# Kernel optimization log

Measured on AMD Instinct MI355X. Metric: run time of the kernel, lower is better.

Reference implementation:

```python
import jax, jax.numpy as jnp
import numpy as np


def setup_inputs() -> dict:
    key = jax.random.key(0)
    k_x, k_q, k_k, k_v = jax.random.split(key, 4)
    seq_len, d_in, d_out = 4096, 1024, 1024
    x = jax.random.normal(k_x, (seq_len, d_in), dtype=jnp.float32)
    # torch nn.Linear weights are [d_out, d_in]; applied as x @ W.T
    scale = 1.0 / np.sqrt(d_in)
    Wq = jax.random.uniform(k_q, (d_out, d_in), jnp.float32, -scale, scale)
    Wk = jax.random.uniform(k_k, (d_out, d_in), jnp.float32, -scale, scale)
    Wv = jax.random.uniform(k_v, (d_out, d_in), jnp.float32, -scale, scale)
    return {"x": x, "Wq": Wq, "Wk": Wk, "Wv": Wv}


def reference(x, Wq, Wk, Wv):
    # x: [S, d_in]; Wq/Wk/Wv: [d_out, d_in]
    queries = x @ Wq.T          # [S, d_out]
    keys = x @ Wk.T             # [S, d_out]
    values = x @ Wv.T           # [S, d_out]
    d_k = keys.shape[-1]
    attn_scores = queries @ keys.T                      # [S, S]
    attn_weights = jax.nn.softmax(attn_scores / jnp.sqrt(jnp.float32(d_k)), axis=-1)
    S = attn_scores.shape[0]
    tril = jnp.tril(jnp.ones((S, S), dtype=attn_weights.dtype))
    masked = tril * attn_weights
    masked_norm = masked / jnp.sum(masked, axis=-1, keepdims=True)
    context_vec = masked_norm @ values                  # [S, d_out]
    return context_vec
```

## Files before the change

### kernel.cpp

```cpp
#include <hip/hip_runtime.h>
#include <hip/hip_bf16.h>


typedef __bf16 bf16_t;
typedef __bf16 bf16x4v __attribute__((ext_vector_type(4)));
typedef __bf16 bf16x8 __attribute__((ext_vector_type(8)));
typedef float f32x4 __attribute__((ext_vector_type(4)));
typedef unsigned char u8;
typedef long long i64_t;

#define AS1 __attribute__((address_space(1)))
#define AS3 __attribute__((address_space(3)))

__device__ __forceinline__ void async_copy16(const void* g, void* l) {
    __builtin_amdgcn_global_load_lds((AS1 void*)(g), (AS3 void*)(l), 16, 0, 0);
}

__device__ __forceinline__ u8 f32_to_fp8(float v) {
    return (u8)(__builtin_amdgcn_cvt_pk_fp8_f32(v, v, 0, false) & 0xff);
}

__device__ __forceinline__ void store_conv(float* p, float v) { *p = v; }
__device__ __forceinline__ void store_conv(bf16_t* p, float v) { *p = (bf16_t)v; }
__device__ __forceinline__ void store_conv(u8* p, float v) { *p = f32_to_fp8(v); }

__device__ __forceinline__ float sum32(const float* p) {
    const f32x4* v = (const f32x4*)p;
    float s = 0.f;
#pragma unroll
    for (int u = 0; u < 8; ++u) {
        f32x4 a = v[u];
        s += a[0] + a[1] + a[2] + a[3];
    }
    return s;
}

template <int EPI, typename OutT>
__device__ __forceinline__ void gemm_tile_bf16(const bf16_t* __restrict__ A, int lda,
                                               const bf16_t* __restrict__ B, int ldb,
                                               OutT* __restrict__ C, int ldc,
                                               int kb0, int kb1, float alpha,
                                               bf16_t* __restrict__ As,
                                               bf16_t* __restrict__ Bs,
                                               const float* __restrict__ inv) {
    constexpr int BK = 64;
    const int tid = threadIdx.x;
    const int lane = tid & 63, wave = tid >> 6;
    const int wm = wave >> 1, wn = wave & 1;
    const int q = lane >> 4, l16 = lane & 15;

    f32x4 acc[4][4] = {};

    const bf16_t* aSrc[4];
    const bf16_t* bSrc[4];
    int ldsOff[4];
#pragma unroll
    for (int it = 0; it < 4; ++it) {
        int c = it * 256 + tid;
        int r = c >> 3, b = c & 7;
        int sb = b ^ (r & 7);
        aSrc[it] = A + (size_t)r * lda + sb * 8;
        bSrc[it] = B + (size_t)r * ldb + sb * 8;
        ldsOff[it] = c * 8;
    }

    for (int kb = kb0; kb < kb1; ++kb) {
        const int k0 = kb * BK;
#pragma unroll
        for (int it = 0; it < 4; ++it) async_copy16(aSrc[it] + k0, &As[ldsOff[it]]);
#pragma unroll
        for (int it = 0; it < 4; ++it) async_copy16(bSrc[it] + k0, &Bs[ldsOff[it]]);
        __syncthreads();

#pragma unroll
        for (int k2 = 0; k2 < 2; ++k2) {
            bf16x8 af[4], bfr[4];
#pragma unroll
            for (int mt = 0; mt < 4; ++mt) {
                int m = wm * 64 + mt * 16 + l16;
                int blk = (k2 * 4 + q) ^ (m & 7);
                af[mt] = *(const bf16x8*)&As[m * BK + blk * 8];
            }
#pragma unroll
            for (int nt = 0; nt < 4; ++nt) {
                int nn = wn * 64 + nt * 16 + l16;
                int blk = (k2 * 4 + q) ^ (nn & 7);
                bfr[nt] = *(const bf16x8*)&Bs[nn * BK + blk * 8];
            }
#pragma unroll
            for (int mt = 0; mt < 4; ++mt)
#pragma unroll
                for (int nt = 0; nt < 4; ++nt)
                    acc[mt][nt] = __builtin_amdgcn_mfma_f32_16x16x32_bf16(
                        af[mt], bfr[nt], acc[mt][nt], 0, 0, 0);
        }
        __syncthreads();
    }

    const int row0 = wm * 64, col0 = wn * 64;
#pragma unroll
    for (int mt = 0; mt < 4; ++mt)
#pragma unroll
        for (int nt = 0; nt < 4; ++nt)
#pragma unroll
            for (int r = 0; r < 4; ++r) {
                int lr = row0 + mt * 16 + q * 4 + r;
                float v = acc[mt][nt][r];
                v = (EPI == 2) ? v * inv[lr] : v * alpha;
                store_conv(&C[(size_t)lr * ldc + col0 + nt * 16 + l16], v);
            }
}

__device__ __forceinline__ void scores_tile_fp8(const u8* __restrict__ A, int lda,
                                                const u8* __restrict__ B, int ldb,
                                                bf16_t* __restrict__ C, int ldc,
                                                float alpha,
                                                u8* __restrict__ As, u8* __restrict__ Bs,
                                                float* __restrict__ partial,
                                                int gr0, int gc0,
                                                float* __restrict__ sred) {
    const int tid = threadIdx.x;
    const int lane = tid & 63, wave = tid >> 6;
    const int wm = wave >> 1, wn = wave & 1;
    const int q = lane >> 4, l16 = lane & 15;

    f32x4 acc[4][4] = {};

    const u8* aSrc[4];
    const u8* bSrc[4];
    int ldsOff[4];
#pragma unroll
    for (int it = 0; it < 4; ++it) {
        int c = it * 256 + tid;
        int r = c >> 3, b = c & 7;
        int sb = b ^ (r & 7);
        aSrc[it] = A + (size_t)r * lda + sb * 16;
        bSrc[it] = B + (size_t)r * ldb + sb * 16;
        ldsOff[it] = c * 16;
    }

    for (int kb = 0; kb < 8; ++kb) {
        const int k0 = kb * 128;
#pragma unroll
        for (int it = 0; it < 4; ++it) async_copy16(aSrc[it] + k0, &As[ldsOff[it]]);
#pragma unroll
        for (int it = 0; it < 4; ++it) async_copy16(bSrc[it] + k0, &Bs[ldsOff[it]]);
        __syncthreads();

#pragma unroll
        for (int k2 = 0; k2 < 4; ++k2) {
            i64_t af[4], bfr[4];
            const int cb = 2 * k2 + (q >> 1), co = (q & 1) * 8;
#pragma unroll
            for (int mt = 0; mt < 4; ++mt) {
                int m = wm * 64 + mt * 16 + l16;
                af[mt] = *(const i64_t*)&As[m * 128 + ((cb ^ (m & 7)) << 4) + co];
            }
#pragma unroll
            for (int nt = 0; nt < 4; ++nt) {
                int nn = wn * 64 + nt * 16 + l16;
                bfr[nt] = *(const i64_t*)&Bs[nn * 128 + ((cb ^ (nn & 7)) << 4) + co];
            }
#pragma unroll
            for (int mt = 0; mt < 4; ++mt)
#pragma unroll
                for (int nt = 0; nt < 4; ++nt)
                    acc[mt][nt] = __builtin_amdgcn_mfma_f32_16x16x32_fp8_fp8(
                        af[mt], bfr[nt], acc[mt][nt], 0, 0, 0);
        }
        __syncthreads();
    }

    const int row0 = wm * 64, col0 = wn * 64;
    float esum[4][4];
#pragma unroll
    for (int mt = 0; mt < 4; ++mt)
#pragma unroll
        for (int r = 0; r < 4; ++r) esum[mt][r] = 0.f;
#pragma unroll
    for (int mt = 0; mt < 4; ++mt)
#pragma unroll
        for (int nt = 0; nt < 4; ++nt)
#pragma unroll
            for (int r = 0; r < 4; ++r) {
                int lr = row0 + mt * 16 + q * 4 + r;
                int lc = col0 + nt * 16 + l16;
                float p = (gc0 + lc > gr0 + lr) ? 0.f : __expf(acc[mt][nt][r] * alpha);
                esum[mt][r] += p;
                C[(size_t)lr * ldc + lc] = (bf16_t)p;
            }
#pragma unroll
    for (int mt = 0; mt < 4; ++mt)
#pragma unroll
        for (int r = 0; r < 4; ++r) {
#pragma unroll
            for (int off = 1; off < 16; off <<= 1)
                esum[mt][r] += __shfl_xor(esum[mt][r], off, 64);
            if (l16 == 0) sred[(row0 + mt * 16 + q * 4 + r) * 2 + wn] = esum[mt][r];
        }
    __syncthreads();
    if (tid < 128) partial[(size_t)tid * 32] = sred[tid * 2] + sred[tid * 2 + 1];
}

__global__ __launch_bounds__(256) void k_qkv(const bf16_t* __restrict__ xb,
                                             const bf16_t* __restrict__ wqk,
                                             u8* __restrict__ qk) {
    __shared__ __attribute__((aligned(16))) bf16_t As[128 * 64];
    __shared__ __attribute__((aligned(16))) bf16_t Bs[128 * 64];
    int b = blockIdx.x;
    int bm = b & 31, bn = b >> 5;
    gemm_tile_bf16<0, u8>(xb + (size_t)bm * 128 * 1024, 1024,
                          wqk + (size_t)bn * 128 * 1024, 1024,
                          qk + (size_t)bm * 128 * 2048 + bn * 128, 2048,
                          0, 16, 1.f, As, Bs, nullptr);
}

__global__ __launch_bounds__(256) void k_sv(const bf16_t* __restrict__ xb,
                                            const bf16_t* __restrict__ wvb,
                                            const u8* __restrict__ qk,
                                            bf16_t* __restrict__ vt,
                                            bf16_t* __restrict__ P,
                                            float* __restrict__ rowsum_part) {
    __shared__ __attribute__((aligned(16))) char smem[33 * 1024 + 1024];
    int b = blockIdx.x;
    if (b < 256) {
        bf16_t* As = (bf16_t*)smem;
        bf16_t* Bs = (bf16_t*)(smem + 16384);
        int bm = b & 7, bn = b >> 3;
        gemm_tile_bf16<0, bf16_t>(wvb + (size_t)bm * 128 * 1024, 1024,
                                  xb + (size_t)bn * 128 * 1024, 1024,
                                  vt + (size_t)bm * 128 * 4096 + bn * 128, 4096,
                                  0, 16, 1.f, As, Bs, nullptr);
        return;
    }
    u8* As = (u8*)smem;
    u8* Bs = (u8*)(smem + 16384);
    float* sred = (float*)(smem + 32768);
    int t = b - 256;
    int bm = (int)((sqrtf(8.f * (float)t + 1.f) - 1.f) * 0.5f);
    while (bm * (bm + 1) / 2 > t) --bm;
    while ((bm + 1) * (bm + 2) / 2 <= t) ++bm;
    int bn = t - bm * (bm + 1) / 2;
    scores_tile_fp8(qk + (size_t)bm * 128 * 2048, 2048,
                    qk + 1024 + (size_t)bn * 128 * 2048, 2048,
                    P + (size_t)bm * 128 * 4096 + bn * 128, 4096,
                    0.03125f, As, Bs,
                    rowsum_part + (size_t)bm * 128 * 32 + bn,
                    bm * 128, bn * 128, sred);
    if (bn == bm) {
        float* rp = rowsum_part + (size_t)bm * 128 * 32;
        int tid = threadIdx.x;
        for (int r = tid >> 4; r < 128; r += 16)
            for (int u = bm + 1 + (tid & 15); u < 32; u += 16)
                rp[r * 32 + u] = 0.f;
    }
}

__global__ __launch_bounds__(256) void k_pv(const bf16_t* __restrict__ P,
                                            const bf16_t* __restrict__ vt,
                                            const float* __restrict__ rowsum_part,
                                            float* __restrict__ out,
                                            float* __restrict__ partials) {
    __shared__ __attribute__((aligned(16))) bf16_t As[128 * 64];
    __shared__ __attribute__((aligned(16))) bf16_t Bs[128 * 64];
    __shared__ float sInv[128];
    int b = blockIdx.x;
    int bn = b & 7, g = b >> 3;
    int bm, s, ns;
    if (g < 8)       { bm = g;                 s = 0;            ns = 1; }
    else if (g < 24) { bm = 8 + (g - 8) / 2;   s = (g - 8) % 2;  ns = 2; }
    else if (g < 48) { bm = 16 + (g - 24) / 3; s = (g - 24) % 3; ns = 3; }
    else             { bm = 24 + (g - 48) / 4; s = (g - 48) % 4; ns = 4; }
    int nk = 2 * (bm + 1);
    int kb0 = s * nk / ns;
    int kb1 = (s + 1) * nk / ns;

    const bf16_t* A = P + (size_t)bm * 128 * 4096;
    const bf16_t* B = vt + (size_t)bn * 128 * 4096;
    if (ns == 1) {
        int tid = threadIdx.x;
        if (tid < 128)
            sInv[tid] = 1.f / sum32(rowsum_part + (size_t)(bm * 128 + tid) * 32);
        gemm_tile_bf16<2, float>(A, 4096, B, 4096,
                                 out + (size_t)bm * 128 * 1024 + bn * 128, 1024,
                                 kb0, kb1, 1.f, As, Bs, sInv);
    } else {
        int cum = (bm < 16) ? (bm - 8) * 2
                : (bm < 24) ? 16 + (bm - 16) * 3
                            : 40 + (bm - 24) * 4;
        gemm_tile_bf16<0, float>(A, 4096, B, 4096,
                                 partials + ((size_t)(cum + s) * 8 + bn) * 16384, 128,
                                 kb0, kb1, 1.f, As, Bs, nullptr);
    }
}

__global__ __launch_bounds__(256) void k_reduce(const float* __restrict__ partials,
                                                const float* __restrict__ rowsum_part,
                                                float* __restrict__ out) {
    int b = blockIdx.x;
    int t = b % 192, p = b / 192;
    int bm = t % 24 + 8, bn = t / 24;
    int ns = (bm < 16) ? 2 : (bm < 24) ? 3 : 4;
    int cum = (bm < 16) ? (bm - 8) * 2
            : (bm < 24) ? 16 + (bm - 16) * 3
                        : 40 + (bm - 24) * 4;
    __shared__ float sInv[8];
    int tid = threadIdx.x;
    if (tid < 8) {
        int row = bm * 128 + p * 8 + tid;
        sInv[tid] = 1.f / sum32(rowsum_part + (size_t)row * 32);
    }
    __syncthreads();

    int idx = p * 1024 + tid * 4;
    int lr = idx >> 7, lc = idx & 127;
    float sx = 0.f, sy = 0.f, sz = 0.f, sw = 0.f;
    for (int u = 0; u < ns; ++u) {
        const float4 v = *(const float4*)(partials + ((size_t)(cum + u) * 8 + bn) * 16384 + idx);
        sx += v.x; sy += v.y; sz += v.z; sw += v.w;
    }
    float inv = sInv[lr - p * 8];
    float4 o = {sx * inv, sy * inv, sz * inv, sw * inv};
    *(float4*)(out + (size_t)(bm * 128 + lr) * 1024 + bn * 128 + lc) = o;
}

__global__ __launch_bounds__(256) void cast_to_bf16(const float* __restrict__ x,
                                                    const float* __restrict__ Wq,
                                                    const float* __restrict__ Wk,
                                                    const float* __restrict__ Wv,
                                                    bf16_t* __restrict__ xb,
                                                    bf16_t* __restrict__ wqk,
                                                    bf16_t* __restrict__ wv) {
    const int NX = (4096 * 1024) / 4;
    const int NW = (1024 * 1024) / 4;
    int idx = blockIdx.x * 256 + threadIdx.x;
    const float* src;
    bf16_t* dst;
    int off;
    if (idx < NX) {
        src = x; dst = xb; off = idx;
    } else if (idx < NX + NW) {
        src = Wq; dst = wqk; off = idx - NX;
    } else if (idx < NX + 2 * NW) {
        src = Wk; dst = wqk + (size_t)NW * 4; off = idx - NX - NW;
    } else {
        src = Wv; dst = wv; off = idx - NX - 2 * NW;
    }
    float4 f = ((const float4*)src)[off];
    bf16x4v o;
    o.x = (bf16_t)f.x; o.y = (bf16_t)f.y; o.z = (bf16_t)f.z; o.w = (bf16_t)f.w;
    *(bf16x4v*)(dst + (size_t)off * 4) = o;
}

extern "C" void kernel_launch(void* const* d_in, const int* in_sizes, int n_in,
                              void* d_out, int out_size, void* d_ws, size_t ws_size,
                              hipStream_t stream) {
    (void)in_sizes; (void)n_in; (void)out_size; (void)ws_size;
    const float* x  = (const float*)d_in[0];
    const float* Wq = (const float*)d_in[1];
    const float* Wk = (const float*)d_in[2];
    const float* Wv = (const float*)d_in[3];
    float* out = (float*)d_out;

    char* ws = (char*)d_ws;
    bf16_t* xb   = (bf16_t*)(ws + (size_t)0);
    bf16_t* wqk  = (bf16_t*)(ws + ((size_t)8 << 20));
    bf16_t* wvb  = (bf16_t*)(ws + ((size_t)12 << 20));
    u8*     qk   = (u8*)(ws + ((size_t)14 << 20));
    bf16_t* vt   = (bf16_t*)(ws + ((size_t)22 << 20));
    bf16_t* P    = (bf16_t*)(ws + ((size_t)30 << 20));
    float* rowsp = (float*)(ws + ((size_t)62 << 20));
    float* parts = (float*)(ws + ((size_t)64 << 20));

    cast_to_bf16<<<7168, 256, 0, stream>>>(x, Wq, Wk, Wv, xb, wqk, wvb);

    k_qkv<<<512, 256, 0, stream>>>(xb, wqk, qk);

    k_sv<<<784, 256, 0, stream>>>(xb, wvb, qk, vt, P, rowsp);

    k_pv<<<640, 256, 0, stream>>>(P, vt, rowsp, out, parts);
    k_reduce<<<3072, 256, 0, stream>>>(parts, rowsp, out);
}
```

Baseline: 188.8 us.

## Double-buffer LDS tiles in GEMM kernels and stage epilogue stores through LDS

The bf16 and fp8 GEMM tile routines now prefetch the next K-block into a second LDS buffer while computing on the current one, so global loads overlap with MFMA work and one barrier per iteration is removed. Epilogues write results into swizzled LDS and then issue coalesced 16-byte global stores instead of scattered scalar stores. LDS per block grows to 64 KB, which may lower occupancy. A wait on the async copies is also dropped, since only the end-of-iteration barrier orders the prefetch.

```diff
diff --git a/kernel.cpp b/kernel.cpp
--- a/kernel.cpp
+++ b/kernel.cpp
@@ -40,10 +40,11 @@
                                                const bf16_t* __restrict__ B, int ldb,
                                                OutT* __restrict__ C, int ldc,
                                                int kb0, int kb1, float alpha,
-                                               bf16_t* __restrict__ As,
-                                               bf16_t* __restrict__ Bs,
+                                               char* __restrict__ smem,
                                                const float* __restrict__ inv) {
     constexpr int BK = 64;
+    bf16_t* As = (bf16_t*)smem;
+    bf16_t* Bs = (bf16_t*)(smem + 32768);
     const int tid = threadIdx.x;
     const int lane = tid & 63, wave = tid >> 6;
     const int wm = wave >> 1, wn = wave & 1;
@@ -64,14 +65,27 @@
         ldsOff[it] = c * 8;
     }
 
+    {
+        const int k0 = kb0 * BK;
+#pragma unroll
+        for (int it = 0; it < 4; ++it) async_copy16(aSrc[it] + k0, &As[ldsOff[it]]);
+#pragma unroll
+        for (int it = 0; it < 4; ++it) async_copy16(bSrc[it] + k0, &Bs[ldsOff[it]]);
+    }
+    __syncthreads();
+
+    int cur = 0;
     for (int kb = kb0; kb < kb1; ++kb) {
-        const int k0 = kb * BK;
-#pragma unroll
-        for (int it = 0; it < 4; ++it) async_copy16(aSrc[it] + k0, &As[ldsOff[it]]);
-#pragma unroll
-        for (int it = 0; it < 4; ++it) async_copy16(bSrc[it] + k0, &Bs[ldsOff[it]]);
-        __syncthreads();
-
+        if (kb + 1 < kb1) {
+            const int k0 = (kb + 1) * BK;
+            const int boff = (cur ^ 1) * 8192;
+#pragma unroll
+            for (int it = 0; it < 4; ++it) async_copy16(aSrc[it] + k0, &As[boff + ldsOff[it]]);
+#pragma unroll
+            for (int it = 0; it < 4; ++it) async_copy16(bSrc[it] + k0, &Bs[boff + ldsOff[it]]);
+        }
+        const bf16_t* Ab = As + cur * 8192;
+        const bf16_t* Bb = Bs + cur * 8192;
 #pragma unroll
         for (int k2 = 0; k2 < 2; ++k2) {
             bf16x8 af[4], bfr[4];
@@ -79,13 +93,13 @@
             for (int mt = 0; mt < 4; ++mt) {
                 int m = wm * 64 + mt * 16 + l16;
                 int blk = (k2 * 4 + q) ^ (m & 7);
-                af[mt] = *(const bf16x8*)&As[m * BK + blk * 8];
+                af[mt] = *(const bf16x8*)&Ab[m * BK + blk * 8];
             }
 #pragma unroll
             for (int nt = 0; nt < 4; ++nt) {
                 int nn = wn * 64 + nt * 16 + l16;
                 int blk = (k2 * 4 + q) ^ (nn & 7);
-                bfr[nt] = *(const bf16x8*)&Bs[nn * BK + blk * 8];
+                bfr[nt] = *(const bf16x8*)&Bb[nn * BK + blk * 8];
             }
 #pragma unroll
             for (int mt = 0; mt < 4; ++mt)
@@ -95,8 +109,11 @@
                         af[mt], bfr[nt], acc[mt][nt], 0, 0, 0);
         }
         __syncthreads();
-    }
-
+        cur ^= 1;
+    }
+
+    constexpr int S = (int)sizeof(OutT);
+    constexpr int RB = 128 * S;
     const int row0 = wm * 64, col0 = wn * 64;
 #pragma unroll
     for (int mt = 0; mt < 4; ++mt)
@@ -105,20 +122,33 @@
 #pragma unroll
             for (int r = 0; r < 4; ++r) {
                 int lr = row0 + mt * 16 + q * 4 + r;
+                int lc = col0 + nt * 16 + l16;
                 float v = acc[mt][nt][r];
                 v = (EPI == 2) ? v * inv[lr] : v * alpha;
-                store_conv(&C[(size_t)lr * ldc + col0 + nt * 16 + l16], v);
-            }
+                int cb = (lc * S) >> 4;
+                int sw = cb ^ ((lr >> 2) & 7);
+                store_conv((OutT*)(smem + lr * RB + (sw << 4) + ((lc * S) & 15)), v);
+            }
+    __syncthreads();
+#pragma unroll
+    for (int p = 0; p < 4 * S; ++p) {
+        int g = p * 4096 + tid * 16;
+        int r = g / RB;
+        int wb = g & (RB - 1);
+        int sc = (wb >> 4) ^ ((r >> 2) & 7);
+        f32x4 val = *(const f32x4*)(smem + r * RB + (sc << 4));
+        *(f32x4*)((char*)C + (size_t)r * ((size_t)ldc * S) + wb) = val;
+    }
 }
 
 __device__ __forceinline__ void scores_tile_fp8(const u8* __restrict__ A, int lda,
                                                 const u8* __restrict__ B, int ldb,
                                                 bf16_t* __restrict__ C, int ldc,
-                                                float alpha,
-                                                u8* __restrict__ As, u8* __restrict__ Bs,
+                                                float alpha, char* __restrict__ smem,
                                                 float* __restrict__ partial,
-                                                int gr0, int gc0,
-                                                float* __restrict__ sred) {
+                                                int gr0, int gc0) {
+    u8* As = (u8*)smem;
+    u8* Bs = (u8*)(smem + 32768);
     const int tid = threadIdx.x;
     const int lane = tid & 63, wave = tid >> 6;
     const int wm = wave >> 1, wn = wave & 1;
@@ -139,14 +169,26 @@
         ldsOff[it] = c * 16;
     }
 
+    {
+#pragma unroll
+        for (int it = 0; it < 4; ++it) async_copy16(aSrc[it], &As[ldsOff[it]]);
+#pragma unroll
+        for (int it = 0; it < 4; ++it) async_copy16(bSrc[it], &Bs[ldsOff[it]]);
+    }
+    __syncthreads();
+
+    int cur = 0;
     for (int kb = 0; kb < 8; ++kb) {
-        const int k0 = kb * 128;
-#pragma unroll
-        for (int it = 0; it < 4; ++it) async_copy16(aSrc[it] + k0, &As[ldsOff[it]]);
-#pragma unroll
-        for (int it = 0; it < 4; ++it) async_copy16(bSrc[it] + k0, &Bs[ldsOff[it]]);
-        __syncthreads();
-
+        if (kb < 7) {
+            const int k0 = (kb + 1) * 128;
+            const int boff = (cur ^ 1) * 16384;
+#pragma unroll
+            for (int it = 0; it < 4; ++it) async_copy16(aSrc[it] + k0, &As[boff + ldsOff[it]]);
+#pragma unroll
+            for (int it = 0; it < 4; ++it) async_copy16(bSrc[it] + k0, &Bs[boff + ldsOff[it]]);
+        }
+        const u8* Ab = As + cur * 16384;
+        const u8* Bb = Bs + cur * 16384;
 #pragma unroll
         for (int k2 = 0; k2 < 4; ++k2) {
             i64_t af[4], bfr[4];
@@ -154,12 +196,12 @@
 #pragma unroll
             for (int mt = 0; mt < 4; ++mt) {
                 int m = wm * 64 + mt * 16 + l16;
-                af[mt] = *(const i64_t*)&As[m * 128 + ((cb ^ (m & 7)) << 4) + co];
+                af[mt] = *(const i64_t*)&Ab[m * 128 + ((cb ^ (m & 7)) << 4) + co];
             }
 #pragma unroll
             for (int nt = 0; nt < 4; ++nt) {
                 int nn = wn * 64 + nt * 16 + l16;
-                bfr[nt] = *(const i64_t*)&Bs[nn * 128 + ((cb ^ (nn & 7)) << 4) + co];
+                bfr[nt] = *(const i64_t*)&Bb[nn * 128 + ((cb ^ (nn & 7)) << 4) + co];
             }
 #pragma unroll
             for (int mt = 0; mt < 4; ++mt)
@@ -169,8 +211,10 @@
                         af[mt], bfr[nt], acc[mt][nt], 0, 0, 0);
         }
         __syncthreads();
-    }
-
+        cur ^= 1;
+    }
+
+    float* sred = (float*)(smem + 32768);
     const int row0 = wm * 64, col0 = wn * 64;
     float esum[4][4];
 #pragma unroll
@@ -185,9 +229,10 @@
             for (int r = 0; r < 4; ++r) {
                 int lr = row0 + mt * 16 + q * 4 + r;
                 int lc = col0 + nt * 16 + l16;
-                float p = (gc0 + lc > gr0 + lr) ? 0.f : __expf(acc[mt][nt][r] * alpha);
-                esum[mt][r] += p;
-                C[(size_t)lr * ldc + lc] = (bf16_t)p;
+                float pe = (gc0 + lc > gr0 + lr) ? 0.f : __expf(acc[mt][nt][r] * alpha);
+                esum[mt][r] += pe;
+                int sw = (lc >> 3) ^ ((lr >> 2) & 7);
+                *(bf16_t*)(smem + lr * 256 + (sw << 4) + ((lc * 2) & 15)) = (bf16_t)pe;
             }
 #pragma unroll
     for (int mt = 0; mt < 4; ++mt)
@@ -199,20 +244,28 @@
             if (l16 == 0) sred[(row0 + mt * 16 + q * 4 + r) * 2 + wn] = esum[mt][r];
         }
     __syncthreads();
+#pragma unroll
+    for (int p = 0; p < 8; ++p) {
+        int g = p * 4096 + tid * 16;
+        int r = g >> 8;
+        int wb = g & 255;
+        int sc = (wb >> 4) ^ ((r >> 2) & 7);
+        f32x4 val = *(const f32x4*)(smem + r * 256 + (sc << 4));
+        *(f32x4*)((char*)C + (size_t)r * ((size_t)ldc * 2) + wb) = val;
+    }
     if (tid < 128) partial[(size_t)tid * 32] = sred[tid * 2] + sred[tid * 2 + 1];
 }
 
 __global__ __launch_bounds__(256) void k_qkv(const bf16_t* __restrict__ xb,
                                              const bf16_t* __restrict__ wqk,
                                              u8* __restrict__ qk) {
-    __shared__ __attribute__((aligned(16))) bf16_t As[128 * 64];
-    __shared__ __attribute__((aligned(16))) bf16_t Bs[128 * 64];
+    __shared__ __attribute__((aligned(16))) char smem[65536];
     int b = blockIdx.x;
     int bm = b & 31, bn = b >> 5;
     gemm_tile_bf16<0, u8>(xb + (size_t)bm * 128 * 1024, 1024,
                           wqk + (size_t)bn * 128 * 1024, 1024,
                           qk + (size_t)bm * 128 * 2048 + bn * 128, 2048,
-                          0, 16, 1.f, As, Bs, nullptr);
+                          0, 16, 1.f, smem, nullptr);
 }
 
 __global__ __launch_bounds__(256) void k_sv(const bf16_t* __restrict__ xb,
@@ -221,21 +274,16 @@
                                             bf16_t* __restrict__ vt,
                                             bf16_t* __restrict__ P,
                                             float* __restrict__ rowsum_part) {
-    __shared__ __attribute__((aligned(16))) char smem[33 * 1024 + 1024];
+    __shared__ __attribute__((aligned(16))) char smem[65536];
     int b = blockIdx.x;
     if (b < 256) {
-        bf16_t* As = (bf16_t*)smem;
-        bf16_t* Bs = (bf16_t*)(smem + 16384);
         int bm = b & 7, bn = b >> 3;
         gemm_tile_bf16<0, bf16_t>(wvb + (size_t)bm * 128 * 1024, 1024,
                                   xb + (size_t)bn * 128 * 1024, 1024,
                                   vt + (size_t)bm * 128 * 4096 + bn * 128, 4096,
-                                  0, 16, 1.f, As, Bs, nullptr);
+                                  0, 16, 1.f, smem, nullptr);
         return;
     }
-    u8* As = (u8*)smem;
-    u8* Bs = (u8*)(smem + 16384);
-    float* sred = (float*)(smem + 32768);
     int t = b - 256;
     int bm = (int)((sqrtf(8.f * (float)t + 1.f) - 1.f) * 0.5f);
     while (bm * (bm + 1) / 2 > t) --bm;
@@ -244,9 +292,9 @@
     scores_tile_fp8(qk + (size_t)bm * 128 * 2048, 2048,
                     qk + 1024 + (size_t)bn * 128 * 2048, 2048,
                     P + (size_t)bm * 128 * 4096 + bn * 128, 4096,
-                    0.03125f, As, Bs,
+                    0.03125f, smem,
                     rowsum_part + (size_t)bm * 128 * 32 + bn,
-                    bm * 128, bn * 128, sred);
+                    bm * 128, bn * 128);
     if (bn == bm) {
         float* rp = rowsum_part + (size_t)bm * 128 * 32;
         int tid = threadIdx.x;
@@ -261,8 +309,7 @@
                                             const float* __restrict__ rowsum_part,
                                             float* __restrict__ out,
                                             float* __restrict__ partials) {
-    __shared__ __attribute__((aligned(16))) bf16_t As[128 * 64];
-    __shared__ __attribute__((aligned(16))) bf16_t Bs[128 * 64];
+    __shared__ __attribute__((aligned(16))) char smem[65536];
     __shared__ float sInv[128];
     int b = blockIdx.x;
     int bn = b & 7, g = b >> 3;
@@ -283,14 +330,14 @@
             sInv[tid] = 1.f / sum32(rowsum_part + (size_t)(bm * 128 + tid) * 32);
         gemm_tile_bf16<2, float>(A, 4096, B, 4096,
                                  out + (size_t)bm * 128 * 1024 + bn * 128, 1024,
-                                 kb0, kb1, 1.f, As, Bs, sInv);
+                                 kb0, kb1, 1.f, smem, sInv);
     } else {
         int cum = (bm < 16) ? (bm - 8) * 2
                 : (bm < 24) ? 16 + (bm - 16) * 3
                             : 40 + (bm - 24) * 4;
         gemm_tile_bf16<0, float>(A, 4096, B, 4096,
                                  partials + ((size_t)(cum + s) * 8 + bn) * 16384, 128,
-                                 kb0, kb1, 1.f, As, Bs, nullptr);
+                                 kb0, kb1, 1.f, smem, nullptr);
     }
 }
 
```

Result: faster. 182.6 us (-3.3%).
